# Optimization experiments

Hardware: AMD Instinct MI355X
Metric: run time of the kernel (lower is better)

The kernel has to match this reference:

```python
import jax, jax.numpy as jnp
import numpy as np

FEATS = 768
HEAD = 12


def _phi(t):
    # elu feature map + 1 (guarantees positivity)
    return jax.nn.elu(t) + 1.0


def setup_inputs() -> dict:
    key = jax.random.key(0)
    ks = jax.random.split(key, 9)
    f = FEATS
    s = 1.0 / np.sqrt(f)
    x = jax.random.normal(ks[0], (4, 4096, f), dtype=jnp.float32)
    # weights stored as [in, out] so projection is x @ W + b
    Wq = jax.random.normal(ks[1], (f, f), dtype=jnp.float32) * s
    bq = jax.random.normal(ks[2], (f,), dtype=jnp.float32) * 0.01
    Wk = jax.random.normal(ks[3], (f, f), dtype=jnp.float32) * s
    bk = jax.random.normal(ks[4], (f,), dtype=jnp.float32) * 0.01
    Wv = jax.random.normal(ks[5], (f, f), dtype=jnp.float32) * s
    bv = jax.random.normal(ks[6], (f,), dtype=jnp.float32) * 0.01
    Wo = jax.random.normal(ks[7], (f, f), dtype=jnp.float32) * s
    bo = jax.random.normal(ks[8], (f,), dtype=jnp.float32) * 0.01
    return {"x": x, "Wq": Wq, "bq": bq, "Wk": Wk, "bk": bk,
            "Wv": Wv, "bv": bv, "Wo": Wo, "bo": bo}


def reference(x, Wq, bq, Wk, bk, Wv, bv, Wo, bo):
    b, n, f = x.shape
    h = HEAD
    d = f // h
    # project and split heads: [b, h, n, d]
    def heads(t):
        return t.reshape(b, n, h, d).transpose(0, 2, 1, 3)
    q = _phi(heads(x @ Wq + bq))
    k = _phi(heads(x @ Wk + bk))
    v = heads(x @ Wv + bv)
    # kv summary: [b, h, d, d] (sum over sequence)
    kv = jnp.einsum('bhnd,bhne->bhde', k, v)
    # normalizer: z[b,h,l] = 1 / (q[b,h,l,:] . sum_n k[b,h,n,:])  (no eps, as in source)
    ksum = k.sum(axis=2)                      # [b, h, d]
    z = 1.0 / jnp.einsum('bhld,bhd->bhl', q, ksum)  # [b, h, n]
    num = jnp.einsum('bhld,bhde->bhle', q, kv)      # [b, h, n, d]
    normed = num * z[..., None]                     # [b, h, n, d]
    out = normed.transpose(0, 2, 1, 3).reshape(b, n, f)  # [b, n, f]
    return out @ Wo + bo  # dropout p=0.0 -> identity
```

## Files before the change

### kernel.cpp

```cpp
#include <hip/hip_runtime.h>
#include <cstdint>
#include <cstddef>

#define DEVI __device__ __forceinline__

typedef short    shortx8 __attribute__((ext_vector_type(8)));
typedef short    shortx4 __attribute__((ext_vector_type(4)));
typedef short    shortx2 __attribute__((ext_vector_type(2)));
typedef __bf16   bf16x8  __attribute__((ext_vector_type(8)));
typedef float    floatx4 __attribute__((ext_vector_type(4)));

DEVI unsigned short f2b(float f) {
    union { float f; unsigned u; } a; a.f = f;
    unsigned r = a.u + 0x7fffu + ((a.u >> 16) & 1u);
    return (unsigned short)(r >> 16);
}
DEVI float b2f(unsigned short u) {
    union { unsigned u; float f; } a; a.u = ((unsigned)u) << 16;
    return a.f;
}

DEVI floatx4 mfma_bf16(bf16x8 a, bf16x8 b, floatx4 c) {
    return __builtin_amdgcn_mfma_f32_16x16x32_bf16(a, b, c, 0, 0, 0);
}

DEVI void glds16(const ushort* g, ushort* l) {
    __builtin_amdgcn_global_load_lds(
        (const __attribute__((address_space(1))) void*)g,
        (__attribute__((address_space(3))) void*)l, 16, 0, 0);
}

__global__ void k_prep(const float* __restrict__ x, ushort* __restrict__ xb,
                       const float* __restrict__ Wq, const float* __restrict__ Wk,
                       const float* __restrict__ Wv, const float* __restrict__ Wo,
                       ushort* __restrict__ Wt, ushort* __restrict__ Wot,
                       const float* __restrict__ bq, const float* __restrict__ bk,
                       const float* __restrict__ bv, float* __restrict__ bqkv) {
    __shared__ float tile[64][65];
    const int bid = blockIdx.x, t = threadIdx.x;
    if (bid < 6144) {
        size_t i = ((size_t)bid * 256 + t) * 8;
        float4 v0 = *(const float4*)(x + i);
        float4 v1 = *(const float4*)(x + i + 4);
        shortx8 o;
        o[0] = (short)f2b(v0.x); o[1] = (short)f2b(v0.y);
        o[2] = (short)f2b(v0.z); o[3] = (short)f2b(v0.w);
        o[4] = (short)f2b(v1.x); o[5] = (short)f2b(v1.y);
        o[6] = (short)f2b(v1.z); o[7] = (short)f2b(v1.w);
        *(shortx8*)(xb + i) = o;
    } else if (bid < 6720) {
        int pid = bid - 6144;
        int zi = pid / 144, rem = pid % 144;
        const float* W = (zi == 0) ? Wq : (zi == 1) ? Wk : (zi == 2) ? Wv : Wo;
        const int i0 = (rem / 12) * 64, j0 = (rem % 12) * 64;
        const int c = t & 63, r4 = t >> 6;
        for (int rr = r4; rr < 64; rr += 4)
            tile[rr][c] = W[(size_t)(i0 + rr) * 768 + j0 + c];
        __syncthreads();
        ushort* dst = (zi < 3) ? (Wt + (size_t)(zi * 768) * 768) : Wot;
        for (int jj = r4; jj < 64; jj += 4)
            dst[(size_t)(j0 + jj) * 768 + i0 + c] = f2b(tile[c][jj]);
    } else {
        int j = (bid - 6720) * 256 + t;
        if (j < 2304) {
            const float* src = (j < 768) ? bq : (j < 1536) ? bk : bv;
            bqkv[j] = src[j % 768];
        }
    }
}

template <int MODE>
__global__ __launch_bounds__(256, 2) void k_gemm(
    const ushort* __restrict__ A, const ushort* __restrict__ Bt,
    const float* __restrict__ bias, void* __restrict__ Cout, int Ncols) {
    constexpr int K = 768;
    __shared__ ushort As[128 * 64];
    __shared__ ushort Bs[128 * 64];
    const int m0 = blockIdx.x * 128;
    const int n0 = blockIdx.y * 128;
    const int tid = threadIdx.x;
    const int w = tid >> 6, lane = tid & 63;

    const int lr = lane >> 3;
    const int lc = ((lane & 7) ^ lr) * 8;
    const ushort* ag[4]; const ushort* bg[4]; ushort* al[4]; ushort* bl[4];
#pragma unroll
    for (int i = 0; i < 4; ++i) {
        ag[i] = A  + (size_t)(m0 + w * 32 + i * 8 + lr) * K + lc;
        bg[i] = Bt + (size_t)(n0 + w * 32 + i * 8 + lr) * K + lc;
        al[i] = As + (w * 32 + i * 8) * 64;
        bl[i] = Bs + (w * 32 + i * 8) * 64;
    }

    const int rBase = (w >> 1) * 64;
    const int nBase = (w & 1) * 64;
    const int fr = lane & 15;
    const int q4 = lane >> 4;

    floatx4 acc[4][4] = {};

    for (int k0 = 0; k0 < K; k0 += 64) {
#pragma unroll
        for (int i = 0; i < 4; ++i) glds16(ag[i] + k0, al[i]);
#pragma unroll
        for (int i = 0; i < 4; ++i) glds16(bg[i] + k0, bl[i]);
        __syncthreads();
#pragma unroll
        for (int kc = 0; kc < 2; ++kc) {
            const int off = ((kc * 4 + q4) ^ (fr & 7)) * 8;
            bf16x8 af[4], bf[4];
#pragma unroll
            for (int rt = 0; rt < 4; ++rt)
                af[rt] = *(const bf16x8*)(As + (rBase + rt * 16 + fr) * 64 + off);
#pragma unroll
            for (int nt = 0; nt < 4; ++nt)
                bf[nt] = *(const bf16x8*)(Bs + (nBase + nt * 16 + fr) * 64 + off);
#pragma unroll
            for (int rt = 0; rt < 4; ++rt)
#pragma unroll
                for (int nt = 0; nt < 4; ++nt)
                    acc[rt][nt] = mfma_bf16(af[rt], bf[nt], acc[rt][nt]);
        }
        __syncthreads();
    }

#pragma unroll
    for (int rt = 0; rt < 4; ++rt) {
#pragma unroll
        for (int nt = 0; nt < 4; ++nt) {
#pragma unroll
            for (int r = 0; r < 4; ++r) {
                int m = m0 + rBase + rt * 16 + q4 * 4 + r;
                int n = n0 + nBase + nt * 16 + fr;
                float v = acc[rt][nt][r] + bias[n];
                if (MODE == 0) {
                    if (n < 1536) v = (v > 0.f) ? (v + 1.f) : __expf(v);
                    ((ushort*)Cout)[(size_t)m * Ncols + n] = f2b(v);
                } else {
                    ((float*)Cout)[(size_t)m * Ncols + n] = v;
                }
            }
        }
    }
}

__global__ __launch_bounds__(256) void k_kv(const ushort* __restrict__ QKV,
                                            float* __restrict__ kvp) {
    const int bh = blockIdx.x, s = blockIdx.y;
    const int bb = bh / 12, head = bh % 12;
    __shared__ ushort kS[64 * 70];
    __shared__ ushort vS[64 * 70];
    const int t = threadIdx.x, w = t >> 6, lane = t & 63;
    const int fr = lane & 15, fk = (lane >> 4) * 8;

    floatx4 acc[5] = {};
    const int n_ld = t >> 2, c16 = (t & 3) * 16;
    const ushort* base = QKV + (size_t)(bb * 4096 + s * 512) * 2304 + 768 + head * 64 + c16;

    for (int rr = 0; rr < 8; ++rr) {
        if (rr) __syncthreads();
        {
            const ushort* kp = base + (size_t)(rr * 64 + n_ld) * 2304;
            union { shortx8 v8; shortx2 v2[4]; } k0, k1, v0, v1;
            k0.v8 = *(const shortx8*)(kp);
            k1.v8 = *(const shortx8*)(kp + 8);
            v0.v8 = *(const shortx8*)(kp + 768);
            v1.v8 = *(const shortx8*)(kp + 776);
            ushort* kd = kS + n_ld * 70 + c16;
            ushort* vd = vS + n_ld * 70 + c16;
#pragma unroll
            for (int i = 0; i < 4; ++i) {
                *(shortx2*)(kd + 2 * i)     = k0.v2[i];
                *(shortx2*)(kd + 8 + 2 * i) = k1.v2[i];
                *(shortx2*)(vd + 2 * i)     = v0.v2[i];
                *(shortx2*)(vd + 8 + 2 * i) = v1.v2[i];
            }
        }
        __syncthreads();
#pragma unroll
        for (int kl = 0; kl < 64; kl += 32) {
            union { bf16x8 v; ushort u[8]; } bfr, afr[4];
#pragma unroll
            for (int i = 0; i < 8; ++i) {
                int n = kl + fk + i;
                bfr.u[i] = kS[n * 70 + w * 16 + fr];
#pragma unroll
                for (int mt = 0; mt < 4; ++mt)
                    afr[mt].u[i] = vS[n * 70 + mt * 16 + fr];
            }
            union { bf16x8 v; ushort u[8]; } ones;
            ushort ov = (fr == 0) ? (ushort)0x3F80 : (ushort)0;
#pragma unroll
            for (int i = 0; i < 8; ++i) ones.u[i] = ov;
#pragma unroll
            for (int mt = 0; mt < 4; ++mt)
                acc[mt] = mfma_bf16(afr[mt].v, bfr.v, acc[mt]);
            acc[4] = mfma_bf16(ones.v, bfr.v, acc[4]);
        }
    }

    float* dst = kvp + ((size_t)bh * 8 + s) * (65 * 64);
#pragma unroll
    for (int mt = 0; mt < 4; ++mt)
#pragma unroll
        for (int r = 0; r < 4; ++r)
            dst[(mt * 16 + (lane >> 4) * 4 + r) * 64 + w * 16 + fr] = acc[mt][r];
    if (lane < 16) dst[64 * 64 + w * 16 + lane] = acc[4][0];
}

__global__ void k_kvred(const float* __restrict__ kvp, ushort* __restrict__ kvb) {
    int t4 = (blockIdx.x * 256 + threadIdx.x) * 4;
    int bh = t4 / 4160, rem = t4 % 4160;
    const float* p = kvp + (size_t)bh * 8 * 4160 + rem;
    float4 sum = {0.f, 0.f, 0.f, 0.f};
    for (int i = 0; i < 8; ++i) {
        float4 a = *(const float4*)(p + (size_t)i * 4160);
        sum.x += a.x; sum.y += a.y; sum.z += a.z; sum.w += a.w;
    }
    shortx4 o;
    o[0] = (short)f2b(sum.x); o[1] = (short)f2b(sum.y);
    o[2] = (short)f2b(sum.z); o[3] = (short)f2b(sum.w);
    *(shortx4*)(kvb + t4) = o;
}

__global__ __launch_bounds__(256) void k_num(const ushort* __restrict__ QKV,
                                             const ushort* __restrict__ kvb,
                                             ushort* __restrict__ normed) {
    const int bh = blockIdx.x, l0 = blockIdx.y * 128;
    const int bb = bh / 12, head = bh % 12;
    __shared__ ushort qsh[128 * 72];
    __shared__ ushort kvT[80 * 72];
    __shared__ float dnm[128];
    const int t = threadIdx.x, w = t >> 6, lane = t & 63;

    {
        const ushort* kvbb = kvb + (size_t)bh * 4160;
        int c8 = (t & 7) * 8;
        for (int r0 = (t >> 3); r0 < 65; r0 += 32)
            *(shortx8*)(kvT + r0 * 72 + c8) = *(const shortx8*)(kvbb + r0 * 64 + c8);
    }
    for (int idx = t; idx < 15 * 72; idx += 256) kvT[65 * 72 + idx] = 0;

    const ushort* qg = QKV + (size_t)(bb * 4096 + l0) * 2304 + head * 64;
    {
        int row = t >> 3, c8 = (t & 7) * 8;
#pragma unroll
        for (int i = 0; i < 4; ++i) {
            shortx8 v = *(const shortx8*)(qg + (size_t)(i * 32 + row) * 2304 + c8);
            *(shortx8*)(qsh + (i * 32 + row) * 72 + c8) = v;
        }
    }
    __syncthreads();

    const int fr = lane & 15, fk = (lane >> 4) * 8;
    floatx4 acc[2][5] = {};
#pragma unroll
    for (int kc = 0; kc < 2; ++kc) {
        bf16x8 a[2], b[5];
#pragma unroll
        for (int rt = 0; rt < 2; ++rt)
            a[rt] = *(const bf16x8*)(qsh + (w * 32 + rt * 16 + fr) * 72 + kc * 32 + fk);
#pragma unroll
        for (int nt = 0; nt < 5; ++nt)
            b[nt] = *(const bf16x8*)(kvT + (nt * 16 + fr) * 72 + kc * 32 + fk);
#pragma unroll
        for (int rt = 0; rt < 2; ++rt)
#pragma unroll
            for (int nt = 0; nt < 5; ++nt)
                acc[rt][nt] = mfma_bf16(a[rt], b[nt], acc[rt][nt]);
    }
    if (fr == 0) {
#pragma unroll
        for (int rt = 0; rt < 2; ++rt)
#pragma unroll
            for (int r = 0; r < 4; ++r)
                dnm[w * 32 + rt * 16 + (lane >> 4) * 4 + r] = acc[rt][4][r];
    }
    __syncthreads();
#pragma unroll
    for (int rt = 0; rt < 2; ++rt) {
#pragma unroll
        for (int r = 0; r < 4; ++r) {
            int ml = w * 32 + rt * 16 + (lane >> 4) * 4 + r;
            float z = 1.f / dnm[ml];
            size_t base = (size_t)(bb * 4096 + l0 + ml) * 768 + head * 64;
#pragma unroll
            for (int nt = 0; nt < 4; ++nt)
                normed[base + nt * 16 + fr] = f2b(acc[rt][nt][r] * z);
        }
    }
}

extern "C" void kernel_launch(void* const* d_in, const int* in_sizes, int n_in,
                              void* d_out, int out_size, void* d_ws, size_t ws_size,
                              hipStream_t stream) {
    const float* x  = (const float*)d_in[0];
    const float* Wq = (const float*)d_in[1];
    const float* bq = (const float*)d_in[2];
    const float* Wk = (const float*)d_in[3];
    const float* bk = (const float*)d_in[4];
    const float* Wv = (const float*)d_in[5];
    const float* bv = (const float*)d_in[6];
    const float* Wo = (const float*)d_in[7];
    const float* bo = (const float*)d_in[8];

    char* ws = (char*)d_ws;
    ushort* Xb   = (ushort*)(ws);
    ushort* Wt   = (ushort*)(ws + 25165824);
    ushort* Wot  = (ushort*)(ws + 28704768);
    float*  bqkv = (float*)(ws + 29884416);
    ushort* QKV  = (ushort*)(ws + 29893632);
    float*  kvp  = (float*)(ws + 105391104);
    ushort* kvb  = (ushort*)(ws + 111780864);
    ushort* normed = Xb;

    k_prep <<<dim3(6729),      256, 0, stream>>>(x, Xb, Wq, Wk, Wv, Wo, Wt, Wot,
                                                 bq, bk, bv, bqkv);
    k_gemm<0><<<dim3(128, 18), 256, 0, stream>>>(Xb, Wt, bqkv, (void*)QKV, 2304);
    k_kv   <<<dim3(48, 8),     256, 0, stream>>>(QKV, kvp);
    k_kvred<<<dim3(195),       256, 0, stream>>>(kvp, kvb);
    k_num  <<<dim3(48, 32),    256, 0, stream>>>(QKV, kvb, normed);
    k_gemm<1><<<dim3(128, 6),  256, 0, stream>>>(normed, Wot, bo, d_out, 768);
}
```

Before: 231.1 us.

## Restructure GEMM into 256x256 double-buffered 8-wave ping-pong pipeline

Rewrites the shared GEMM kernel to use 256x256 output tiles computed by 512 threads (8 waves), with double-buffered LDS. Global-to-LDS loads for the next K tile are split into quarters and interleaved with four MFMA phases. Explicit waitcnt, barriers and s_setprio steer the schedule so memory traffic overlaps compute. The larger tiles raise operand reuse and cut barrier overhead per FLOP. In exchange, LDS use grows to 128 KB per block, and the grid shrinks (192 blocks for the output projection), which risks leaving CUs idle and causing tail imbalance.

```diff
diff --git a/kernel.cpp b/kernel.cpp
--- a/kernel.cpp
+++ b/kernel.cpp
@@ -29,6 +29,13 @@
         (const __attribute__((address_space(1))) void*)g,
         (__attribute__((address_space(3))) void*)l, 16, 0, 0);
 }
+
+DEVI void barrier_f() {
+    __builtin_amdgcn_s_barrier();
+    asm volatile("" ::: "memory");
+}
+
+template <bool B> struct BoolT { static constexpr bool value = B; };
 
 __global__ void k_prep(const float* __restrict__ x, ushort* __restrict__ xb,
                        const float* __restrict__ Wq, const float* __restrict__ Wk,
@@ -70,69 +77,171 @@
 }
 
 template <int MODE>
-__global__ __launch_bounds__(256, 2) void k_gemm(
+__global__ __launch_bounds__(512, 2) void k_gemm(
     const ushort* __restrict__ A, const ushort* __restrict__ Bt,
     const float* __restrict__ bias, void* __restrict__ Cout, int Ncols) {
     constexpr int K = 768;
-    __shared__ ushort As[128 * 64];
-    __shared__ ushort Bs[128 * 64];
-    const int m0 = blockIdx.x * 128;
-    const int n0 = blockIdx.y * 128;
+    constexpr int NKT = K / 64;
+    __shared__ ushort As[2][256 * 64];
+    __shared__ ushort Bs[2][256 * 64];
+    const int m0 = blockIdx.x * 256;
+    const int n0 = blockIdx.y * 256;
     const int tid = threadIdx.x;
     const int w = tid >> 6, lane = tid & 63;
-
-    const int lr = lane >> 3;
-    const int lc = ((lane & 7) ^ lr) * 8;
-    const ushort* ag[4]; const ushort* bg[4]; ushort* al[4]; ushort* bl[4];
-#pragma unroll
-    for (int i = 0; i < 4; ++i) {
-        ag[i] = A  + (size_t)(m0 + w * 32 + i * 8 + lr) * K + lc;
-        bg[i] = Bt + (size_t)(n0 + w * 32 + i * 8 + lr) * K + lc;
-        al[i] = As + (w * 32 + i * 8) * 64;
-        bl[i] = Bs + (w * 32 + i * 8) * 64;
-    }
-
-    const int rBase = (w >> 1) * 64;
-    const int nBase = (w & 1) * 64;
-    const int fr = lane & 15;
-    const int q4 = lane >> 4;
-
-    floatx4 acc[4][4] = {};
-
-    for (int k0 = 0; k0 < K; k0 += 64) {
-#pragma unroll
-        for (int i = 0; i < 4; ++i) glds16(ag[i] + k0, al[i]);
-#pragma unroll
-        for (int i = 0; i < 4; ++i) glds16(bg[i] + k0, bl[i]);
-        __syncthreads();
+    const int wm = w >> 2, wn = w & 3;
+    const int lr = lane >> 3, ls = lane & 7;
+    const int lc = (ls ^ lr) * 8;
+    const int fr = lane & 15, q4 = lane >> 4;
+
+    const ushort* gA = A  + (size_t)(m0 + w * 8 + lr) * K + lc;
+    const ushort* gB = Bt + (size_t)(n0 + (w >> 2) * 64 + (w & 3) * 8 + lr) * K + lc;
+    const int aOfs = (w * 8) * 64;
+    const int bOfs = ((w >> 2) * 64 + (w & 3) * 8) * 64;
+
+    floatx4 acc[8][4] = {};
+
+    glds16(gA,           As[0] + aOfs);
+    glds16(gA + 128 * K, As[0] + 128 * 64 + aOfs);
+    glds16(gB,           Bs[0] + bOfs);
+    glds16(gB + 128 * K, Bs[0] + 128 * 64 + bOfs);
+    glds16(gB + 32 * K,  Bs[0] + 32 * 64 + bOfs);
+    glds16(gB + 160 * K, Bs[0] + 160 * 64 + bOfs);
+    glds16(gA + 64 * K,  As[0] + 64 * 64 + aOfs);
+    glds16(gA + 192 * K, As[0] + 192 * 64 + aOfs);
+    asm volatile("s_waitcnt vmcnt(4)" ::: "memory");
+    barrier_f();
+
+    auto tile = [&](int kt, auto stc) {
+        constexpr bool ST = decltype(stc)::value;
+        const int cur = kt & 1;
+        const ushort* a_ = As[cur];
+        const ushort* b_ = Bs[cur];
+        ushort* An = As[cur ^ 1];
+        ushort* Bn = Bs[cur ^ 1];
+        const int ko = (kt + 1) * 64;
+        bf16x8 af[2][4], bfv[2][2][2];
+
 #pragma unroll
         for (int kc = 0; kc < 2; ++kc) {
             const int off = ((kc * 4 + q4) ^ (fr & 7)) * 8;
-            bf16x8 af[4], bf[4];
-#pragma unroll
-            for (int rt = 0; rt < 4; ++rt)
-                af[rt] = *(const bf16x8*)(As + (rBase + rt * 16 + fr) * 64 + off);
-#pragma unroll
-            for (int nt = 0; nt < 4; ++nt)
-                bf[nt] = *(const bf16x8*)(Bs + (nBase + nt * 16 + fr) * 64 + off);
-#pragma unroll
-            for (int rt = 0; rt < 4; ++rt)
-#pragma unroll
-                for (int nt = 0; nt < 4; ++nt)
-                    acc[rt][nt] = mfma_bf16(af[rt], bf[nt], acc[rt][nt]);
-        }
-        __syncthreads();
-    }
-
-#pragma unroll
-    for (int rt = 0; rt < 4; ++rt) {
-#pragma unroll
-        for (int nt = 0; nt < 4; ++nt) {
+#pragma unroll
+            for (int rt = 0; rt < 4; ++rt)
+                af[kc][rt] = *(const bf16x8*)(a_ + (wm * 128 + rt * 16 + fr) * 64 + off);
+#pragma unroll
+            for (int nt = 0; nt < 2; ++nt)
+                bfv[0][kc][nt] = *(const bf16x8*)(b_ + (wn * 64 + nt * 16 + fr) * 64 + off);
+        }
+        if constexpr (ST) {
+            glds16(gA + ko,           An + aOfs);
+            glds16(gA + 128 * K + ko, An + 128 * 64 + aOfs);
+        }
+        barrier_f();
+        asm volatile("s_waitcnt lgkmcnt(0)" ::: "memory");
+        __builtin_amdgcn_sched_barrier(0);
+        __builtin_amdgcn_s_setprio(1);
+#pragma unroll
+        for (int kc = 0; kc < 2; ++kc)
+#pragma unroll
+            for (int rt = 0; rt < 4; ++rt)
+#pragma unroll
+                for (int nt = 0; nt < 2; ++nt)
+                    acc[rt][nt] = mfma_bf16(af[kc][rt], bfv[0][kc][nt], acc[rt][nt]);
+        __builtin_amdgcn_s_setprio(0);
+        if constexpr (ST) asm volatile("s_waitcnt vmcnt(4)" ::: "memory");
+        else              asm volatile("s_waitcnt vmcnt(2)" ::: "memory");
+        barrier_f();
+
+#pragma unroll
+        for (int kc = 0; kc < 2; ++kc) {
+            const int off = ((kc * 4 + q4) ^ (fr & 7)) * 8;
+#pragma unroll
+            for (int nt = 0; nt < 2; ++nt)
+                bfv[1][kc][nt] = *(const bf16x8*)(b_ + (wn * 64 + 32 + nt * 16 + fr) * 64 + off);
+        }
+        if constexpr (ST) {
+            glds16(gB + ko,           Bn + bOfs);
+            glds16(gB + 128 * K + ko, Bn + 128 * 64 + bOfs);
+        }
+        barrier_f();
+        asm volatile("s_waitcnt lgkmcnt(0)" ::: "memory");
+        __builtin_amdgcn_sched_barrier(0);
+        __builtin_amdgcn_s_setprio(1);
+#pragma unroll
+        for (int kc = 0; kc < 2; ++kc)
+#pragma unroll
+            for (int rt = 0; rt < 4; ++rt)
+#pragma unroll
+                for (int nt = 0; nt < 2; ++nt)
+                    acc[rt][2 + nt] = mfma_bf16(af[kc][rt], bfv[1][kc][nt], acc[rt][2 + nt]);
+        __builtin_amdgcn_s_setprio(0);
+        if constexpr (ST) asm volatile("s_waitcnt vmcnt(4)" ::: "memory");
+        else              asm volatile("s_waitcnt vmcnt(0)" ::: "memory");
+        barrier_f();
+
+#pragma unroll
+        for (int kc = 0; kc < 2; ++kc) {
+            const int off = ((kc * 4 + q4) ^ (fr & 7)) * 8;
+#pragma unroll
+            for (int rt = 0; rt < 4; ++rt)
+                af[kc][rt] = *(const bf16x8*)(a_ + (wm * 128 + 64 + rt * 16 + fr) * 64 + off);
+        }
+        if constexpr (ST) {
+            glds16(gB + 32 * K + ko,  Bn + 32 * 64 + bOfs);
+            glds16(gB + 160 * K + ko, Bn + 160 * 64 + bOfs);
+        }
+        barrier_f();
+        asm volatile("s_waitcnt lgkmcnt(0)" ::: "memory");
+        __builtin_amdgcn_sched_barrier(0);
+        __builtin_amdgcn_s_setprio(1);
+#pragma unroll
+        for (int kc = 0; kc < 2; ++kc)
+#pragma unroll
+            for (int rt = 0; rt < 4; ++rt)
+#pragma unroll
+                for (int nt = 0; nt < 2; ++nt)
+                    acc[4 + rt][nt] = mfma_bf16(af[kc][rt], bfv[0][kc][nt], acc[4 + rt][nt]);
+        __builtin_amdgcn_s_setprio(0);
+        if constexpr (ST) {
+            asm volatile("s_waitcnt vmcnt(4)" ::: "memory");
+            barrier_f();
+        }
+
+        if constexpr (ST) {
+            glds16(gA + 64 * K + ko,  An + 64 * 64 + aOfs);
+            glds16(gA + 192 * K + ko, An + 192 * 64 + aOfs);
+            barrier_f();
+        }
+        __builtin_amdgcn_s_setprio(1);
+#pragma unroll
+        for (int kc = 0; kc < 2; ++kc)
+#pragma unroll
+            for (int rt = 0; rt < 4; ++rt)
+#pragma unroll
+                for (int nt = 0; nt < 2; ++nt)
+                    acc[4 + rt][2 + nt] = mfma_bf16(af[kc][rt], bfv[1][kc][nt], acc[4 + rt][2 + nt]);
+        __builtin_amdgcn_s_setprio(0);
+        if constexpr (ST) {
+            asm volatile("s_waitcnt vmcnt(4)" ::: "memory");
+            barrier_f();
+        }
+    };
+
+#pragma unroll 1
+    for (int kt = 0; kt < NKT - 1; ++kt) tile(kt, BoolT<true>{});
+    tile(NKT - 1, BoolT<false>{});
+
+    float bv[4];
+#pragma unroll
+    for (int ni = 0; ni < 4; ++ni) bv[ni] = bias[n0 + wn * 64 + ni * 16 + fr];
+#pragma unroll
+    for (int mi = 0; mi < 8; ++mi) {
+#pragma unroll
+        for (int ni = 0; ni < 4; ++ni) {
 #pragma unroll
             for (int r = 0; r < 4; ++r) {
-                int m = m0 + rBase + rt * 16 + q4 * 4 + r;
-                int n = n0 + nBase + nt * 16 + fr;
-                float v = acc[rt][nt][r] + bias[n];
+                const int m = m0 + wm * 128 + mi * 16 + q4 * 4 + r;
+                const int n = n0 + wn * 64 + ni * 16 + fr;
+                float v = acc[mi][ni][r] + bv[ni];
                 if (MODE == 0) {
                     if (n < 1536) v = (v > 0.f) ? (v + 1.f) : __expf(v);
                     ((ushort*)Cout)[(size_t)m * Ncols + n] = f2b(v);
@@ -314,11 +423,11 @@
     ushort* kvb  = (ushort*)(ws + 111780864);
     ushort* normed = Xb;
 
-    k_prep <<<dim3(6729),      256, 0, stream>>>(x, Xb, Wq, Wk, Wv, Wo, Wt, Wot,
-                                                 bq, bk, bv, bqkv);
-    k_gemm<0><<<dim3(128, 18), 256, 0, stream>>>(Xb, Wt, bqkv, (void*)QKV, 2304);
-    k_kv   <<<dim3(48, 8),     256, 0, stream>>>(QKV, kvp);
-    k_kvred<<<dim3(195),       256, 0, stream>>>(kvp, kvb);
-    k_num  <<<dim3(48, 32),    256, 0, stream>>>(QKV, kvb, normed);
-    k_gemm<1><<<dim3(128, 6),  256, 0, stream>>>(normed, Wot, bo, d_out, 768);
-}
+    k_prep <<<dim3(6729),     256, 0, stream>>>(x, Xb, Wq, Wk, Wv, Wo, Wt, Wot,
+                                                bq, bk, bv, bqkv);
+    k_gemm<0><<<dim3(64, 9),  512, 0, stream>>>(Xb, Wt, bqkv, (void*)QKV, 2304);
+    k_kv   <<<dim3(48, 8),    256, 0, stream>>>(QKV, kvp);
+    k_kvred<<<dim3(195),      256, 0, stream>>>(kvp, kvb);
+    k_num  <<<dim3(48, 32),   256, 0, stream>>>(QKV, kvb, normed);
+    k_gemm<1><<<dim3(64, 3),  512, 0, stream>>>(normed, Wot, bo, d_out, 768);
+}
```

After: 244.5 us. 1.06x slower.
